# Optimization experiments

Hardware: AMD Instinct MI355X
Metric: run time of the kernel (lower is better)

## Reference

```python
import jax, jax.numpy as jnp
import numpy as np

GAMMA = 1.0
INF_REPLACE = 1e10  # original code replaces inf with 1e10 before logsumexp


def _softmin3(r_diag, r_up, r_left, gamma):
    # softmin over the 3 DP neighbors (stack order matches original: diag, up, left)
    x = jnp.stack([r_diag, r_up, r_left], axis=0)  # (3, B)
    x = jnp.where(jnp.isinf(x), jnp.asarray(INF_REPLACE, x.dtype), x)
    return -gamma * jax.nn.logsumexp(-x / gamma, axis=0)  # (B,)


def _cdist(X, Y):
    # Euclidean pairwise distance, torch.cdist(p=2): (B,N,d),(B,M,d) -> (B,N,M)
    d2 = (jnp.sum(X * X, axis=-1)[:, :, None]
          + jnp.sum(Y * Y, axis=-1)[:, None, :]
          - 2.0 * jnp.einsum('bnd,bmd->bnm', X, Y))
    return jnp.sqrt(jnp.maximum(d2, 0.0))


def _soft_dtw(X, Y, gamma):
    B, N, _ = X.shape
    D = _cdist(X, Y)  # (B, N, N)
    inf = jnp.asarray(jnp.inf, D.dtype)

    # R row 0: [0, inf, inf, ...] per batch
    prev_row0 = jnp.full((B, N + 1), inf, dtype=D.dtype).at[:, 0].set(0.0)

    def row_step(prev_row, d_row):
        # prev_row: (B, N+1) = R[i-1, :]; d_row: (B, N) = D[:, i-1, :]
        xs = (d_row.T, prev_row[:, :-1].T, prev_row[:, 1:].T)  # each (N, B)

        def col_step(r_left, x):
            d, r_diag, r_up = x  # each (B,)
            r = d + _softmin3(r_diag, r_up, r_left, gamma)
            return r, r

        _, row = jax.lax.scan(col_step, jnp.full((B,), inf, dtype=D.dtype), xs)
        new_row = jnp.concatenate([jnp.full((B, 1), inf, dtype=D.dtype), row.T], axis=1)
        return new_row, None

    last_row, _ = jax.lax.scan(row_step, prev_row0, jnp.swapaxes(D, 0, 1))
    return last_row[:, -1]  # R[:, N, N], shape (B,)


def setup_inputs() -> dict:
    key = jax.random.key(0)
    kx, ky = jax.random.split(key)
    B, N, d = 64, 512, 64
    X = jax.random.normal(kx, (B, N, d), dtype=jnp.float32)
    Y = jax.random.normal(ky, (B, N, d), dtype=jnp.float32)
    return {"X": X, "Y": Y}


def reference(X, Y):
    return _soft_dtw(X, Y, GAMMA)
```

## Files before the change

### kernel.cpp

```cpp
#include <hip/hip_runtime.h>
#include <math.h>

#define NB 64
#define NN 512
#define ND 64

#define LOG2E 1.4426950408889634f
#define LN2   0.6931471805599453f
#define RING  16
#define NINF  __int_as_float(0xFF800000u)

typedef __attribute__((ext_vector_type(8))) short  bf16x8;
typedef __attribute__((ext_vector_type(4))) float  f32x4;

static __device__ __forceinline__ unsigned short f2bf(float f) {
    unsigned u = __float_as_uint(f);
    u += 0x7FFFu + ((u >> 16) & 1u);
    return (unsigned short)(u >> 16);
}

__global__ __launch_bounds__(256) void pack_kernel(const float* __restrict__ X,
                                                   const float* __restrict__ Y,
                                                   unsigned short* __restrict__ Xp,
                                                   unsigned short* __restrict__ Yp,
                                                   float* __restrict__ nx,
                                                   float* __restrict__ ny) {
    const int gid = blockIdx.x * 256 + threadIdx.x;
    const float* src;
    unsigned short* dst;
    float* ndst;
    if (blockIdx.y == 0) { src = X + (size_t)gid * ND; dst = Xp; ndst = nx; }
    else                 { src = Y + (size_t)gid * ND; dst = Yp; ndst = ny; }

    float v[ND];
    float s = 0.f;
    #pragma unroll
    for (int k = 0; k < ND; k += 4) {
        float4 f = *(const float4*)(src + k);
        v[k] = f.x; v[k + 1] = f.y; v[k + 2] = f.z; v[k + 3] = f.w;
        s += f.x * f.x + f.y * f.y + f.z * f.z + f.w * f.w;
    }
    ndst[gid] = s;

    const int b  = gid >> 9;
    const int i  = gid & 511;
    const int it = i >> 4;
    const int lm = i & 15;
    #pragma unroll
    for (int h = 0; h < 2; ++h) {
        #pragma unroll
        for (int q = 0; q < 4; ++q) {
            unsigned w[4];
            #pragma unroll
            for (int m = 0; m < 4; ++m) {
                const int c = h * 32 + q * 8 + 2 * m;
                w[m] = (unsigned)f2bf(v[c]) | ((unsigned)f2bf(v[c + 1]) << 16);
            }
            uint4 pkt; pkt.x = w[0]; pkt.y = w[1]; pkt.z = w[2]; pkt.w = w[3];
            *(uint4*)(dst + ((((size_t)b * 32 + it) * 2 + h) << 9)
                          + (size_t)(q * 16 + lm) * 8) = pkt;
        }
    }
}

__global__ __launch_bounds__(256) void cdist_kernel(const unsigned short* __restrict__ Xp,
                                                    const unsigned short* __restrict__ Yp,
                                                    const float* __restrict__ nx,
                                                    const float* __restrict__ ny,
                                                    unsigned short* __restrict__ Wt) {
    const int b  = blockIdx.z;
    const int ib = blockIdx.x * 128;
    const int jb = blockIdx.y * 128;
    const int t  = threadIdx.x;

    const int wave = t >> 6;
    const int wi   = (wave & 1) * 64;
    const int wj   = (wave >> 1) * 64;
    const int lane = t & 63;
    const int lm   = lane & 15;
    const int quad = lane >> 4;

    f32x4 acc[4][4];
    #pragma unroll
    for (int mt = 0; mt < 4; ++mt)
        #pragma unroll
        for (int nt = 0; nt < 4; ++nt)
            acc[mt][nt] = (f32x4){0.f, 0.f, 0.f, 0.f};

    const int jt0 = (jb + wj) >> 4;
    const int it0 = (ib + wi) >> 4;

    #pragma unroll
    for (int h = 0; h < 2; ++h) {
        bf16x8 Af[4], Bf[4];
        #pragma unroll
        for (int mt = 0; mt < 4; ++mt)
            Af[mt] = *(const bf16x8*)(Yp
                + ((((size_t)b * 32 + jt0 + mt) * 2 + h) << 9) + (size_t)lane * 8);
        #pragma unroll
        for (int nt = 0; nt < 4; ++nt)
            Bf[nt] = *(const bf16x8*)(Xp
                + ((((size_t)b * 32 + it0 + nt) * 2 + h) << 9) + (size_t)lane * 8);
        #pragma unroll
        for (int mt = 0; mt < 4; ++mt)
            #pragma unroll
            for (int nt = 0; nt < 4; ++nt)
                acc[mt][nt] = __builtin_amdgcn_mfma_f32_16x16x32_bf16(
                    Af[mt], Bf[nt], acc[mt][nt], 0, 0, 0);
    }

    float nxv[4];
    float4 nyv[4];
    #pragma unroll
    for (int nt = 0; nt < 4; ++nt)
        nxv[nt] = nx[(size_t)b * NN + ib + wi + nt * 16 + lm];
    #pragma unroll
    for (int mt = 0; mt < 4; ++mt)
        nyv[mt] = *(const float4*)(ny + (size_t)b * NN + jb + wj + mt * 16 + quad * 4);

    #pragma unroll
    for (int nt = 0; nt < 4; ++nt) {
        const int i = ib + wi + nt * 16 + lm;
        unsigned short* Drow = Wt + ((size_t)b * NN + i) * NN + jb + wj;
        #pragma unroll
        for (int mt = 0; mt < 4; ++mt) {
            const float* nyp = (const float*)&nyv[mt];
            unsigned a[4];
            #pragma unroll
            for (int r = 0; r < 4; ++r) {
                float d2 = nyp[r] + nxv[nt] - 2.0f * acc[mt][nt][r];
                float w  = __builtin_amdgcn_exp2f(16.0f - LOG2E * sqrtf(fmaxf(d2, 0.f)));
                a[r] = __float_as_uint(w) + 0x8000u;
            }
            uint2 pkt;
            pkt.x = (a[0] >> 16) | (a[1] & 0xFFFF0000u);
            pkt.y = (a[2] >> 16) | (a[3] & 0xFFFF0000u);
            *(uint2*)(Drow + mt * 16 + quad * 4) = pkt;
        }
    }
}

static __device__ __forceinline__ float dpp_shr1(float x, float old) {
    return __int_as_float(__builtin_amdgcn_update_dpp(
        __float_as_int(old), __float_as_int(x), 0x138, 0xf, 0xf, false));
}
static __device__ __forceinline__ float dpp_shl1(float x) {
    return __int_as_float(__builtin_amdgcn_update_dpp(
        0, __float_as_int(x), 0x130, 0xf, 0xf, false));
}

static __device__ __forceinline__ void dtw_step4(
    bool W1, bool DOACT, bool DOGUARD, bool DOCLAMP, bool DOREN,
    int ss, int u, int t, const unsigned short* __restrict__ Wb, int ib,
    uint2* ring, float* L, float& diagHold, float& h, float& Otf,
    float& hbuf, float* __restrict__ h0)
{
    float recvH = dpp_shr1(h, NINF);
    if (W1) {
        recvH = (t == 0) ? hbuf : recvH;
        hbuf  = dpp_shl1(hbuf);
    }
    if (DOACT) { if (ss == t && (t > 0 || W1)) Otf = -recvH; }

    const float up0   = __builtin_amdgcn_exp2f(fminf(recvH + Otf, 80.0f));
    const float diag0 = diagHold;
    diagHold = up0 * 65536.0f;

    const int j = ss - t + 1;
    const uint2 c = ring[u];

    {
        int jn = j + RING;
        if (DOCLAMP) jn = jn < 1 ? 1 : jn;
        ring[u] = *(const uint2*)(Wb + (size_t)(jn - 1) * NN + ib);
    }

    bool act = true;
    if (DOGUARD) act = (j >= 1) && (j <= NN);
    if (act) {
        float dd[4];
        dd[0] = __uint_as_float(c.x << 16);
        dd[1] = __uint_as_float(c.x & 0xFFFF0000u);
        dd[2] = __uint_as_float(c.y << 16);
        dd[3] = __uint_as_float(c.y & 0xFFFF0000u);

        float pre[4], cc[4];
        pre[0] = diag0 + L[0];
        #pragma unroll
        for (int k = 1; k < 4; ++k)
            pre[k] = fmaf(65536.0f, L[k - 1], L[k]);
        #pragma unroll
        for (int k = 0; k < 4; ++k) cc[k] = dd[k] * pre[k];
        float r = up0;
        #pragma unroll
        for (int k = 0; k < 4; ++k) {
            r = fmaf(dd[k], r, cc[k]);
            L[k] = r;
        }

        if (DOREN) {
            float m4 = fmaxf(fmaxf(L[0], L[1]), fmaxf(L[2], L[3]));
            const int   e  = (int)(__float_as_uint(m4) >> 23) - 127;
            const float sc = __uint_as_float((unsigned)(127 - e) << 23);
            #pragma unroll
            for (int k = 0; k < 4; ++k) L[k] *= sc;
            diagHold *= sc;
            Otf -= (float)e;
        }

        h = __builtin_amdgcn_logf(L[3]) - Otf;
        if (!W1) h0[j] = h;
    }
}

static __device__ __forceinline__ void run_chunk(
    bool W1, bool ACT, bool GUARD, bool CLAMP, int base,
    int t, const unsigned short* __restrict__ Wb, int ib,
    uint2* ring, float* L, float& diagHold, float& h, float& Otf,
    float& hbuf, float* __restrict__ h0)
{
    for (int sb = 0; sb < 64; sb += RING)
        #pragma unroll
        for (int u = 0; u < RING; ++u)
            dtw_step4(W1, ACT, GUARD, CLAMP, (u & 1) == 1,
                      base + sb + u, u, t, Wb, ib, ring, L,
                      diagHold, h, Otf, hbuf, h0);
}

__global__ __launch_bounds__(128) void dtw_kernel(const unsigned short* __restrict__ Wt,
                                                  float* __restrict__ out) {
    __shared__ float h0[584];
    const int b    = blockIdx.x;
    const int tid  = threadIdx.x;
    const int t    = tid & 63;
    const int wave = tid >> 6;
    const unsigned short* __restrict__ Wb = Wt + (size_t)b * NN * NN;
    const int ib = wave * 256 + 4 * t;

    float L[4] = {0.f, 0.f, 0.f, 0.f};
    float diagHold = (wave == 0 && t == 0) ? 65536.0f : 0.0f;
    float h = NINF, Otf = 0.0f, hbuf = NINF;

    uint2 ring[RING];
    #pragma unroll
    for (int u = 0; u < RING; ++u) {
        int col = u - t + 1;
        col = col < 1 ? 1 : col;
        ring[u] = *(const uint2*)(Wb + (size_t)(col - 1) * NN + ib);
    }

    for (int wall = 0; wall < 11; ++wall) {
        const int ch = wave ? wall - 2 : wall;
        if (wave == 0) {
            if (ch == 0)
                run_chunk(false, true,  true,  true,  0,      t, Wb, ib, ring, L, diagHold, h, Otf, hbuf, h0);
            else if (ch >= 1 && ch <= 7)
                run_chunk(false, false, false, false, ch*64,  t, Wb, ib, ring, L, diagHold, h, Otf, hbuf, h0);
            else if (ch == 8)
                run_chunk(false, false, true,  false, 512,    t, Wb, ib, ring, L, diagHold, h, Otf, hbuf, h0);
        } else {
            if (ch == 0)
                run_chunk(true,  true,  true,  true,  0,      t, Wb, ib, ring, L, diagHold, h, Otf, hbuf, h0);
            else if (ch >= 1 && ch <= 7)
                run_chunk(true,  false, false, false, ch*64,  t, Wb, ib, ring, L, diagHold, h, Otf, hbuf, h0);
            else if (ch == 8)
                run_chunk(true,  false, true,  false, 512,    t, Wb, ib, ring, L, diagHold, h, Otf, hbuf, h0);
        }
        __syncthreads();
        if (wave && wall >= 1 && wall <= 9)
            hbuf = h0[(wall - 1) * 64 + 1 + t];
    }

    if (wave == 1 && t == 63) out[b] = (16384.0f - h) * LN2;
}

extern "C" void kernel_launch(void* const* d_in, const int* in_sizes, int n_in,
                              void* d_out, int out_size, void* d_ws, size_t ws_size,
                              hipStream_t stream) {
    const float* X = (const float*)d_in[0];
    const float* Y = (const float*)d_in[1];
    float* out = (float*)d_out;

    char* ws = (char*)d_ws;
    unsigned short* Wt = (unsigned short*)(ws);
    unsigned short* Xp = (unsigned short*)(ws + (33554432));
    unsigned short* Yp = (unsigned short*)(ws + (33554432 + 4194304));
    float* nx = (float*)(ws + (33554432 + 2 * 4194304));
    float* ny = (float*)(ws + (33554432 + 2 * 4194304 + 131072));

    pack_kernel<<<dim3(NB * NN / 256, 2), 256, 0, stream>>>(X, Y, Xp, Yp, nx, ny);
    cdist_kernel<<<dim3(4, 4, NB), 256, 0, stream>>>(Xp, Yp, nx, ny, Wt);
    dtw_kernel<<<NB, 128, 0, stream>>>(Wt, out);
}
```

Baseline: 145.7 us.

## Store cost matrix in anti-diagonal skewed layout for coalesced DTW wavefront loads

The cdist kernel now writes the exp-weighted cost matrix into a per-wave skewed layout indexed by wavefront step, so each lane's ring-buffer load in the DTW kernel reads consecutive uint2 elements across lanes. This replaces strided row-wise gathers (one 512-element row stride per lane) with fully coalesced loads and removes the clamp logic. The price is a larger workspace with padding and scattered, less coalesced stores in the cdist epilogue; unwritten padding slots are read but masked by the existing guards.

```diff
diff --git a/kernel.cpp b/kernel.cpp
--- a/kernel.cpp
+++ b/kernel.cpp
@@ -8,6 +8,7 @@
 #define LOG2E 1.4426950408889634f
 #define LN2   0.6931471805599453f
 #define RING  16
+#define SD    592
 #define NINF  __int_as_float(0xFF800000u)
 
 typedef __attribute__((ext_vector_type(8))) short  bf16x8;
@@ -67,7 +68,7 @@
                                                     const unsigned short* __restrict__ Yp,
                                                     const float* __restrict__ nx,
                                                     const float* __restrict__ ny,
-                                                    unsigned short* __restrict__ Wt) {
+                                                    uint2* __restrict__ Wd) {
     const int b  = blockIdx.z;
     const int ib = blockIdx.x * 128;
     const int jb = blockIdx.y * 128;
@@ -121,9 +122,11 @@
     #pragma unroll
     for (int nt = 0; nt < 4; ++nt) {
         const int i = ib + wi + nt * 16 + lm;
-        unsigned short* Drow = Wt + ((size_t)b * NN + i) * NN + jb + wj;
         #pragma unroll
         for (int mt = 0; mt < 4; ++mt) {
+            const int j0 = jb + wj + mt * 16 + quad * 4;
+            const int wv = j0 >> 8;
+            const int tt = (j0 >> 2) & 63;
             const float* nyp = (const float*)&nyv[mt];
             unsigned a[4];
             #pragma unroll
@@ -135,7 +138,7 @@
             uint2 pkt;
             pkt.x = (a[0] >> 16) | (a[1] & 0xFFFF0000u);
             pkt.y = (a[2] >> 16) | (a[3] & 0xFFFF0000u);
-            *(uint2*)(Drow + mt * 16 + quad * 4) = pkt;
+            Wd[((size_t)(b * 2 + wv) * SD + (size_t)(i + tt)) * 64 + tt] = pkt;
         }
     }
 }
@@ -150,8 +153,8 @@
 }
 
 static __device__ __forceinline__ void dtw_step4(
-    bool W1, bool DOACT, bool DOGUARD, bool DOCLAMP, bool DOREN,
-    int ss, int u, int t, const unsigned short* __restrict__ Wb, int ib,
+    bool W1, bool DOACT, bool DOGUARD, bool DOREN,
+    int ss, int u, int t, const uint2* __restrict__ Wdw,
     uint2* ring, float* L, float& diagHold, float& h, float& Otf,
     float& hbuf, float* __restrict__ h0)
 {
@@ -169,11 +172,7 @@
     const int j = ss - t + 1;
     const uint2 c = ring[u];
 
-    {
-        int jn = j + RING;
-        if (DOCLAMP) jn = jn < 1 ? 1 : jn;
-        ring[u] = *(const uint2*)(Wb + (size_t)(jn - 1) * NN + ib);
-    }
+    ring[u] = Wdw[(size_t)(ss + RING) * 64];
 
     bool act = true;
     if (DOGUARD) act = (j >= 1) && (j <= NN);
@@ -214,28 +213,27 @@
 }
 
 static __device__ __forceinline__ void run_chunk(
-    bool W1, bool ACT, bool GUARD, bool CLAMP, int base,
-    int t, const unsigned short* __restrict__ Wb, int ib,
+    bool W1, bool ACT, bool GUARD, int base,
+    int t, const uint2* __restrict__ Wdw,
     uint2* ring, float* L, float& diagHold, float& h, float& Otf,
     float& hbuf, float* __restrict__ h0)
 {
     for (int sb = 0; sb < 64; sb += RING)
         #pragma unroll
         for (int u = 0; u < RING; ++u)
-            dtw_step4(W1, ACT, GUARD, CLAMP, (u & 1) == 1,
-                      base + sb + u, u, t, Wb, ib, ring, L,
+            dtw_step4(W1, ACT, GUARD, (u & 1) == 1,
+                      base + sb + u, u, t, Wdw, ring, L,
                       diagHold, h, Otf, hbuf, h0);
 }
 
-__global__ __launch_bounds__(128) void dtw_kernel(const unsigned short* __restrict__ Wt,
+__global__ __launch_bounds__(128) void dtw_kernel(const uint2* __restrict__ Wd,
                                                   float* __restrict__ out) {
     __shared__ float h0[584];
     const int b    = blockIdx.x;
     const int tid  = threadIdx.x;
     const int t    = tid & 63;
     const int wave = tid >> 6;
-    const unsigned short* __restrict__ Wb = Wt + (size_t)b * NN * NN;
-    const int ib = wave * 256 + 4 * t;
+    const uint2* __restrict__ Wdw = Wd + ((size_t)(b * 2 + wave) * SD) * 64 + t;
 
     float L[4] = {0.f, 0.f, 0.f, 0.f};
     float diagHold = (wave == 0 && t == 0) ? 65536.0f : 0.0f;
@@ -243,28 +241,25 @@
 
     uint2 ring[RING];
     #pragma unroll
-    for (int u = 0; u < RING; ++u) {
-        int col = u - t + 1;
-        col = col < 1 ? 1 : col;
-        ring[u] = *(const uint2*)(Wb + (size_t)(col - 1) * NN + ib);
-    }
+    for (int u = 0; u < RING; ++u)
+        ring[u] = Wdw[(size_t)u * 64];
 
     for (int wall = 0; wall < 11; ++wall) {
         const int ch = wave ? wall - 2 : wall;
         if (wave == 0) {
             if (ch == 0)
-                run_chunk(false, true,  true,  true,  0,      t, Wb, ib, ring, L, diagHold, h, Otf, hbuf, h0);
+                run_chunk(false, true,  true,  0,      t, Wdw, ring, L, diagHold, h, Otf, hbuf, h0);
             else if (ch >= 1 && ch <= 7)
-                run_chunk(false, false, false, false, ch*64,  t, Wb, ib, ring, L, diagHold, h, Otf, hbuf, h0);
+                run_chunk(false, false, false, ch*64,  t, Wdw, ring, L, diagHold, h, Otf, hbuf, h0);
             else if (ch == 8)
-                run_chunk(false, false, true,  false, 512,    t, Wb, ib, ring, L, diagHold, h, Otf, hbuf, h0);
+                run_chunk(false, false, true,  512,    t, Wdw, ring, L, diagHold, h, Otf, hbuf, h0);
         } else {
             if (ch == 0)
-                run_chunk(true,  true,  true,  true,  0,      t, Wb, ib, ring, L, diagHold, h, Otf, hbuf, h0);
+                run_chunk(true,  true,  true,  0,      t, Wdw, ring, L, diagHold, h, Otf, hbuf, h0);
             else if (ch >= 1 && ch <= 7)
-                run_chunk(true,  false, false, false, ch*64,  t, Wb, ib, ring, L, diagHold, h, Otf, hbuf, h0);
+                run_chunk(true,  false, false, ch*64,  t, Wdw, ring, L, diagHold, h, Otf, hbuf, h0);
             else if (ch == 8)
-                run_chunk(true,  false, true,  false, 512,    t, Wb, ib, ring, L, diagHold, h, Otf, hbuf, h0);
+                run_chunk(true,  false, true,  512,    t, Wdw, ring, L, diagHold, h, Otf, hbuf, h0);
         }
         __syncthreads();
         if (wave && wall >= 1 && wall <= 9)
@@ -282,13 +277,13 @@
     float* out = (float*)d_out;
 
     char* ws = (char*)d_ws;
-    unsigned short* Wt = (unsigned short*)(ws);
-    unsigned short* Xp = (unsigned short*)(ws + (33554432));
-    unsigned short* Yp = (unsigned short*)(ws + (33554432 + 4194304));
-    float* nx = (float*)(ws + (33554432 + 2 * 4194304));
-    float* ny = (float*)(ws + (33554432 + 2 * 4194304 + 131072));
+    uint2* Wd = (uint2*)ws;
+    unsigned short* Xp = (unsigned short*)(ws + 41943040);
+    unsigned short* Yp = (unsigned short*)(ws + 41943040 + 4194304);
+    float* nx = (float*)(ws + 41943040 + 2 * 4194304);
+    float* ny = (float*)(ws + 41943040 + 2 * 4194304 + 131072);
 
     pack_kernel<<<dim3(NB * NN / 256, 2), 256, 0, stream>>>(X, Y, Xp, Yp, nx, ny);
-    cdist_kernel<<<dim3(4, 4, NB), 256, 0, stream>>>(Xp, Yp, nx, ny, Wt);
-    dtw_kernel<<<NB, 128, 0, stream>>>(Wt, out);
-}
+    cdist_kernel<<<dim3(4, 4, NB), 256, 0, stream>>>(Xp, Yp, nx, ny, Wd);
+    dtw_kernel<<<NB, 128, 0, stream>>>(Wd, out);
+}
```

Measured after the change: 143.4 us. Within noise of the previous version (-1.6%).

## Split DTW wavefront across four waves with two rows per lane

Applied to the files above, without the earlier changes.

The DTW recurrence is distributed over four waves per block instead of two, with each lane owning two rows of R rather than four. Each wave publishes its boundary row into a dedicated shared-memory buffer for the next wave, and the pipeline skew extends the loop to 15 chunk walls. This cuts the serial per-step arithmetic per lane but adds more pipeline fill/drain steps and barriers.

```diff
diff --git a/kernel.cpp b/kernel.cpp
--- a/kernel.cpp
+++ b/kernel.cpp
@@ -149,129 +149,128 @@
         0, __float_as_int(x), 0x130, 0xf, 0xf, false));
 }
 
-static __device__ __forceinline__ void dtw_step4(
-    bool W1, bool DOACT, bool DOGUARD, bool DOCLAMP, bool DOREN,
+static __device__ __forceinline__ void dtw_step2(
+    bool SUB, bool PUB, bool DOACT, bool DOGUARD, bool DOCLAMP, bool DOREN,
     int ss, int u, int t, const unsigned short* __restrict__ Wb, int ib,
-    uint2* ring, float* L, float& diagHold, float& h, float& Otf,
-    float& hbuf, float* __restrict__ h0)
+    unsigned* ring, float* L, float& diagHold, float& h, float& Otf,
+    float& hbuf, float* __restrict__ h0w)
 {
     float recvH = dpp_shr1(h, NINF);
-    if (W1) {
+    if (SUB) {
         recvH = (t == 0) ? hbuf : recvH;
         hbuf  = dpp_shl1(hbuf);
     }
-    if (DOACT) { if (ss == t && (t > 0 || W1)) Otf = -recvH; }
+    if (DOACT) { if (ss == t && (t > 0 || SUB)) Otf = -recvH; }
 
     const float up0   = __builtin_amdgcn_exp2f(fminf(recvH + Otf, 80.0f));
     const float diag0 = diagHold;
     diagHold = up0 * 65536.0f;
 
     const int j = ss - t + 1;
-    const uint2 c = ring[u];
+    const unsigned c = ring[u];
 
     {
         int jn = j + RING;
         if (DOCLAMP) jn = jn < 1 ? 1 : jn;
-        ring[u] = *(const uint2*)(Wb + (size_t)(jn - 1) * NN + ib);
+        ring[u] = *(const unsigned*)(Wb + (size_t)(jn - 1) * NN + ib);
     }
 
     bool act = true;
     if (DOGUARD) act = (j >= 1) && (j <= NN);
     if (act) {
-        float dd[4];
-        dd[0] = __uint_as_float(c.x << 16);
-        dd[1] = __uint_as_float(c.x & 0xFFFF0000u);
-        dd[2] = __uint_as_float(c.y << 16);
-        dd[3] = __uint_as_float(c.y & 0xFFFF0000u);
-
-        float pre[4], cc[4];
-        pre[0] = diag0 + L[0];
-        #pragma unroll
-        for (int k = 1; k < 4; ++k)
-            pre[k] = fmaf(65536.0f, L[k - 1], L[k]);
-        #pragma unroll
-        for (int k = 0; k < 4; ++k) cc[k] = dd[k] * pre[k];
-        float r = up0;
-        #pragma unroll
-        for (int k = 0; k < 4; ++k) {
-            r = fmaf(dd[k], r, cc[k]);
-            L[k] = r;
-        }
+        const float dd0 = __uint_as_float(c << 16);
+        const float dd1 = __uint_as_float(c & 0xFFFF0000u);
+
+        const float pre0 = diag0 + L[0];
+        const float pre1 = fmaf(65536.0f, L[0], L[1]);
+        const float cc0  = dd0 * pre0;
+        const float cc1  = dd1 * pre1;
+        float r = fmaf(dd0, up0, cc0);
+        L[0] = r;
+        r = fmaf(dd1, r, cc1);
+        L[1] = r;
 
         if (DOREN) {
-            float m4 = fmaxf(fmaxf(L[0], L[1]), fmaxf(L[2], L[3]));
-            const int   e  = (int)(__float_as_uint(m4) >> 23) - 127;
+            const float m2 = fmaxf(L[0], L[1]);
+            const int   e  = (int)(__float_as_uint(m2) >> 23) - 127;
             const float sc = __uint_as_float((unsigned)(127 - e) << 23);
-            #pragma unroll
-            for (int k = 0; k < 4; ++k) L[k] *= sc;
+            L[0] *= sc; L[1] *= sc;
             diagHold *= sc;
             Otf -= (float)e;
         }
 
-        h = __builtin_amdgcn_logf(L[3]) - Otf;
-        if (!W1) h0[j] = h;
+        h = __builtin_amdgcn_logf(L[1]) - Otf;
+        if (PUB) h0w[j] = h;
     }
 }
 
 static __device__ __forceinline__ void run_chunk(
-    bool W1, bool ACT, bool GUARD, bool CLAMP, int base,
+    bool SUB, bool PUB, bool ACT, bool GUARD, bool CLAMP, int base,
     int t, const unsigned short* __restrict__ Wb, int ib,
-    uint2* ring, float* L, float& diagHold, float& h, float& Otf,
-    float& hbuf, float* __restrict__ h0)
+    unsigned* ring, float* L, float& diagHold, float& h, float& Otf,
+    float& hbuf, float* __restrict__ h0w)
 {
     for (int sb = 0; sb < 64; sb += RING)
         #pragma unroll
         for (int u = 0; u < RING; ++u)
-            dtw_step4(W1, ACT, GUARD, CLAMP, (u & 1) == 1,
+            dtw_step2(SUB, PUB, ACT, GUARD, CLAMP, (u & 1) == 1,
                       base + sb + u, u, t, Wb, ib, ring, L,
-                      diagHold, h, Otf, hbuf, h0);
-}
-
-__global__ __launch_bounds__(128) void dtw_kernel(const unsigned short* __restrict__ Wt,
+                      diagHold, h, Otf, hbuf, h0w);
+}
+
+__global__ __launch_bounds__(256) void dtw_kernel(const unsigned short* __restrict__ Wt,
                                                   float* __restrict__ out) {
-    __shared__ float h0[584];
+    __shared__ float h0[3][584];
     const int b    = blockIdx.x;
     const int tid  = threadIdx.x;
     const int t    = tid & 63;
     const int wave = tid >> 6;
     const unsigned short* __restrict__ Wb = Wt + (size_t)b * NN * NN;
-    const int ib = wave * 256 + 4 * t;
-
-    float L[4] = {0.f, 0.f, 0.f, 0.f};
+    const int ib = wave * 128 + 2 * t;
+
+    float L[2] = {0.f, 0.f};
     float diagHold = (wave == 0 && t == 0) ? 65536.0f : 0.0f;
     float h = NINF, Otf = 0.0f, hbuf = NINF;
-
-    uint2 ring[RING];
+    float* h0w = h0[wave < 3 ? wave : 0];
+
+    unsigned ring[RING];
     #pragma unroll
     for (int u = 0; u < RING; ++u) {
         int col = u - t + 1;
         col = col < 1 ? 1 : col;
-        ring[u] = *(const uint2*)(Wb + (size_t)(col - 1) * NN + ib);
-    }
-
-    for (int wall = 0; wall < 11; ++wall) {
-        const int ch = wave ? wall - 2 : wall;
+        ring[u] = *(const unsigned*)(Wb + (size_t)(col - 1) * NN + ib);
+    }
+
+    for (int wall = 0; wall < 15; ++wall) {
+        const int ch = wall - 2 * wave;
         if (wave == 0) {
             if (ch == 0)
-                run_chunk(false, true,  true,  true,  0,      t, Wb, ib, ring, L, diagHold, h, Otf, hbuf, h0);
+                run_chunk(false, true,  true,  true,  true,  0,     t, Wb, ib, ring, L, diagHold, h, Otf, hbuf, h0w);
             else if (ch >= 1 && ch <= 7)
-                run_chunk(false, false, false, false, ch*64,  t, Wb, ib, ring, L, diagHold, h, Otf, hbuf, h0);
+                run_chunk(false, true,  false, false, false, ch*64, t, Wb, ib, ring, L, diagHold, h, Otf, hbuf, h0w);
             else if (ch == 8)
-                run_chunk(false, false, true,  false, 512,    t, Wb, ib, ring, L, diagHold, h, Otf, hbuf, h0);
+                run_chunk(false, true,  false, true,  false, 512,   t, Wb, ib, ring, L, diagHold, h, Otf, hbuf, h0w);
+        } else if (wave < 3) {
+            if (ch == 0)
+                run_chunk(true,  true,  true,  true,  true,  0,     t, Wb, ib, ring, L, diagHold, h, Otf, hbuf, h0w);
+            else if (ch >= 1 && ch <= 7)
+                run_chunk(true,  true,  false, false, false, ch*64, t, Wb, ib, ring, L, diagHold, h, Otf, hbuf, h0w);
+            else if (ch == 8)
+                run_chunk(true,  true,  false, true,  false, 512,   t, Wb, ib, ring, L, diagHold, h, Otf, hbuf, h0w);
         } else {
             if (ch == 0)
-                run_chunk(true,  true,  true,  true,  0,      t, Wb, ib, ring, L, diagHold, h, Otf, hbuf, h0);
+                run_chunk(true,  false, true,  true,  true,  0,     t, Wb, ib, ring, L, diagHold, h, Otf, hbuf, h0w);
             else if (ch >= 1 && ch <= 7)
-                run_chunk(true,  false, false, false, ch*64,  t, Wb, ib, ring, L, diagHold, h, Otf, hbuf, h0);
+                run_chunk(true,  false, false, false, false, ch*64, t, Wb, ib, ring, L, diagHold, h, Otf, hbuf, h0w);
             else if (ch == 8)
-                run_chunk(true,  false, true,  false, 512,    t, Wb, ib, ring, L, diagHold, h, Otf, hbuf, h0);
+                run_chunk(true,  false, false, true,  false, 512,   t, Wb, ib, ring, L, diagHold, h, Otf, hbuf, h0w);
         }
         __syncthreads();
-        if (wave && wall >= 1 && wall <= 9)
-            hbuf = h0[(wall - 1) * 64 + 1 + t];
-    }
-
-    if (wave == 1 && t == 63) out[b] = (16384.0f - h) * LN2;
+        if (wave > 0 && wall >= 2 * wave - 1 && wall <= 2 * wave + 7)
+            hbuf = h0[wave - 1][(wall - 2 * wave + 1) * 64 + 1 + t];
+    }
+
+    if (wave == 3 && t == 63) out[b] = (16384.0f - h) * LN2;
 }
 
 extern "C" void kernel_launch(void* const* d_in, const int* in_sizes, int n_in,
@@ -290,5 +289,5 @@
 
     pack_kernel<<<dim3(NB * NN / 256, 2), 256, 0, stream>>>(X, Y, Xp, Yp, nx, ny);
     cdist_kernel<<<dim3(4, 4, NB), 256, 0, stream>>>(Xp, Yp, nx, ny, Wt);
-    dtw_kernel<<<NB, 128, 0, stream>>>(Wt, out);
-}
+    dtw_kernel<<<NB, 256, 0, stream>>>(Wt, out);
+}
```

New measurement: 177.8 us. 1.22x slower.

## Run soft-DTW wavefront in a single wave with eight rows per lane

Applied to the files above, without the earlier changes.

Each batch's DP now runs in one 64-lane wave, with each lane owning 8 rows instead of 4. This removes the two-wave split, along with its LDS handoff of boundary values and the per-chunk __syncthreads barriers. The wave pipeline now runs 8 chunks plus a tail, not 11 staggered walls. In exchange, each lane's serial dependency chain per step doubles, and only 64 wavefronts are active across the GPU.

```diff
diff --git a/kernel.cpp b/kernel.cpp
--- a/kernel.cpp
+++ b/kernel.cpp
@@ -144,134 +144,109 @@
     return __int_as_float(__builtin_amdgcn_update_dpp(
         __float_as_int(old), __float_as_int(x), 0x138, 0xf, 0xf, false));
 }
-static __device__ __forceinline__ float dpp_shl1(float x) {
-    return __int_as_float(__builtin_amdgcn_update_dpp(
-        0, __float_as_int(x), 0x130, 0xf, 0xf, false));
-}
-
-static __device__ __forceinline__ void dtw_step4(
-    bool W1, bool DOACT, bool DOGUARD, bool DOCLAMP, bool DOREN,
+
+static __device__ __forceinline__ void dtw_step8(
+    bool DOACT, bool DOGUARD, bool DOCLAMP, bool DOREN,
     int ss, int u, int t, const unsigned short* __restrict__ Wb, int ib,
-    uint2* ring, float* L, float& diagHold, float& h, float& Otf,
-    float& hbuf, float* __restrict__ h0)
+    uint4* ring, float* L, float& diagHold, float& h, float& Otf)
 {
-    float recvH = dpp_shr1(h, NINF);
-    if (W1) {
-        recvH = (t == 0) ? hbuf : recvH;
-        hbuf  = dpp_shl1(hbuf);
-    }
-    if (DOACT) { if (ss == t && (t > 0 || W1)) Otf = -recvH; }
+    const float recvH = dpp_shr1(h, NINF);
+    if (DOACT) { if (ss == t && t > 0) Otf = -recvH; }
 
     const float up0   = __builtin_amdgcn_exp2f(fminf(recvH + Otf, 80.0f));
     const float diag0 = diagHold;
     diagHold = up0 * 65536.0f;
 
     const int j = ss - t + 1;
-    const uint2 c = ring[u];
+    const uint4 c = ring[u];
 
     {
         int jn = j + RING;
         if (DOCLAMP) jn = jn < 1 ? 1 : jn;
-        ring[u] = *(const uint2*)(Wb + (size_t)(jn - 1) * NN + ib);
+        ring[u] = *(const uint4*)(Wb + (size_t)(jn - 1) * NN + ib);
     }
 
     bool act = true;
     if (DOGUARD) act = (j >= 1) && (j <= NN);
     if (act) {
-        float dd[4];
+        float dd[8];
         dd[0] = __uint_as_float(c.x << 16);
         dd[1] = __uint_as_float(c.x & 0xFFFF0000u);
         dd[2] = __uint_as_float(c.y << 16);
         dd[3] = __uint_as_float(c.y & 0xFFFF0000u);
-
-        float pre[4], cc[4];
+        dd[4] = __uint_as_float(c.z << 16);
+        dd[5] = __uint_as_float(c.z & 0xFFFF0000u);
+        dd[6] = __uint_as_float(c.w << 16);
+        dd[7] = __uint_as_float(c.w & 0xFFFF0000u);
+
+        float pre[8], cc[8];
         pre[0] = diag0 + L[0];
         #pragma unroll
-        for (int k = 1; k < 4; ++k)
+        for (int k = 1; k < 8; ++k)
             pre[k] = fmaf(65536.0f, L[k - 1], L[k]);
         #pragma unroll
-        for (int k = 0; k < 4; ++k) cc[k] = dd[k] * pre[k];
+        for (int k = 0; k < 8; ++k) cc[k] = dd[k] * pre[k];
         float r = up0;
         #pragma unroll
-        for (int k = 0; k < 4; ++k) {
+        for (int k = 0; k < 8; ++k) {
             r = fmaf(dd[k], r, cc[k]);
             L[k] = r;
         }
 
         if (DOREN) {
-            float m4 = fmaxf(fmaxf(L[0], L[1]), fmaxf(L[2], L[3]));
-            const int   e  = (int)(__float_as_uint(m4) >> 23) - 127;
+            float m01 = fmaxf(L[0], L[1]), m23 = fmaxf(L[2], L[3]);
+            float m45 = fmaxf(L[4], L[5]), m67 = fmaxf(L[6], L[7]);
+            float m8  = fmaxf(fmaxf(m01, m23), fmaxf(m45, m67));
+            const int   e  = (int)(__float_as_uint(m8) >> 23) - 127;
             const float sc = __uint_as_float((unsigned)(127 - e) << 23);
             #pragma unroll
-            for (int k = 0; k < 4; ++k) L[k] *= sc;
+            for (int k = 0; k < 8; ++k) L[k] *= sc;
             diagHold *= sc;
             Otf -= (float)e;
         }
 
-        h = __builtin_amdgcn_logf(L[3]) - Otf;
-        if (!W1) h0[j] = h;
-    }
-}
-
-static __device__ __forceinline__ void run_chunk(
-    bool W1, bool ACT, bool GUARD, bool CLAMP, int base,
+        h = __builtin_amdgcn_logf(L[7]) - Otf;
+    }
+}
+
+static __device__ __forceinline__ void run_chunk8(
+    bool ACT, bool GUARD, bool CLAMP, int base,
     int t, const unsigned short* __restrict__ Wb, int ib,
-    uint2* ring, float* L, float& diagHold, float& h, float& Otf,
-    float& hbuf, float* __restrict__ h0)
+    uint4* ring, float* L, float& diagHold, float& h, float& Otf)
 {
     for (int sb = 0; sb < 64; sb += RING)
         #pragma unroll
         for (int u = 0; u < RING; ++u)
-            dtw_step4(W1, ACT, GUARD, CLAMP, (u & 1) == 1,
+            dtw_step8(ACT, GUARD, CLAMP, (u & 1) == 1,
                       base + sb + u, u, t, Wb, ib, ring, L,
-                      diagHold, h, Otf, hbuf, h0);
-}
-
-__global__ __launch_bounds__(128) void dtw_kernel(const unsigned short* __restrict__ Wt,
-                                                  float* __restrict__ out) {
-    __shared__ float h0[584];
-    const int b    = blockIdx.x;
-    const int tid  = threadIdx.x;
-    const int t    = tid & 63;
-    const int wave = tid >> 6;
+                      diagHold, h, Otf);
+}
+
+__global__ __launch_bounds__(64) void dtw_kernel(const unsigned short* __restrict__ Wt,
+                                                 float* __restrict__ out) {
+    const int b = blockIdx.x;
+    const int t = threadIdx.x;
     const unsigned short* __restrict__ Wb = Wt + (size_t)b * NN * NN;
-    const int ib = wave * 256 + 4 * t;
-
-    float L[4] = {0.f, 0.f, 0.f, 0.f};
-    float diagHold = (wave == 0 && t == 0) ? 65536.0f : 0.0f;
-    float h = NINF, Otf = 0.0f, hbuf = NINF;
-
-    uint2 ring[RING];
+    const int ib = 8 * t;
+
+    float L[8] = {0.f, 0.f, 0.f, 0.f, 0.f, 0.f, 0.f, 0.f};
+    float diagHold = (t == 0) ? 65536.0f : 0.0f;
+    float h = NINF, Otf = 0.0f;
+
+    uint4 ring[RING];
     #pragma unroll
     for (int u = 0; u < RING; ++u) {
         int col = u - t + 1;
         col = col < 1 ? 1 : col;
-        ring[u] = *(const uint2*)(Wb + (size_t)(col - 1) * NN + ib);
-    }
-
-    for (int wall = 0; wall < 11; ++wall) {
-        const int ch = wave ? wall - 2 : wall;
-        if (wave == 0) {
-            if (ch == 0)
-                run_chunk(false, true,  true,  true,  0,      t, Wb, ib, ring, L, diagHold, h, Otf, hbuf, h0);
-            else if (ch >= 1 && ch <= 7)
-                run_chunk(false, false, false, false, ch*64,  t, Wb, ib, ring, L, diagHold, h, Otf, hbuf, h0);
-            else if (ch == 8)
-                run_chunk(false, false, true,  false, 512,    t, Wb, ib, ring, L, diagHold, h, Otf, hbuf, h0);
-        } else {
-            if (ch == 0)
-                run_chunk(true,  true,  true,  true,  0,      t, Wb, ib, ring, L, diagHold, h, Otf, hbuf, h0);
-            else if (ch >= 1 && ch <= 7)
-                run_chunk(true,  false, false, false, ch*64,  t, Wb, ib, ring, L, diagHold, h, Otf, hbuf, h0);
-            else if (ch == 8)
-                run_chunk(true,  false, true,  false, 512,    t, Wb, ib, ring, L, diagHold, h, Otf, hbuf, h0);
-        }
-        __syncthreads();
-        if (wave && wall >= 1 && wall <= 9)
-            hbuf = h0[(wall - 1) * 64 + 1 + t];
-    }
-
-    if (wave == 1 && t == 63) out[b] = (16384.0f - h) * LN2;
+        ring[u] = *(const uint4*)(Wb + (size_t)(col - 1) * NN + ib);
+    }
+
+    run_chunk8(true, true, true, 0, t, Wb, ib, ring, L, diagHold, h, Otf);
+    for (int chunk = 1; chunk <= 7; ++chunk)
+        run_chunk8(false, false, false, chunk * 64, t, Wb, ib, ring, L, diagHold, h, Otf);
+    run_chunk8(false, true, false, 512, t, Wb, ib, ring, L, diagHold, h, Otf);
+
+    if (t == 63) out[b] = (16384.0f - h) * LN2;
 }
 
 extern "C" void kernel_launch(void* const* d_in, const int* in_sizes, int n_in,
@@ -290,5 +265,5 @@
 
     pack_kernel<<<dim3(NB * NN / 256, 2), 256, 0, stream>>>(X, Y, Xp, Yp, nx, ny);
     cdist_kernel<<<dim3(4, 4, NB), 256, 0, stream>>>(Xp, Yp, nx, ny, Wt);
-    dtw_kernel<<<NB, 128, 0, stream>>>(Wt, out);
-}
+    dtw_kernel<<<NB, 64, 0, stream>>>(Wt, out);
+}
```

Measured after the change: 150.0 us. 2.9% more time.
